# Kernel optimization log

Measured on AMD Instinct MI355X. Metric: run time of the kernel, lower is better.

The kernel has to match this reference:

```python
import jax, jax.numpy as jnp
import numpy as np

F_DIM = 128


def setup_inputs() -> dict:
    key = jax.random.key(0)
    ks = jax.random.split(key, 10)
    n_atoms = 50000
    n_edges = 500000
    F = F_DIM
    q = jax.random.normal(ks[0], (n_atoms, 1, F), dtype=jnp.float32)
    mu = jax.random.normal(ks[1], (n_atoms, 3, F), dtype=jnp.float32)
    Wij = jax.random.normal(ks[2], (n_edges, 1, 3 * F), dtype=jnp.float32)
    dir_ij = jax.random.normal(ks[3], (n_edges, 3), dtype=jnp.float32)
    idx_i = jax.random.randint(ks[4], (n_edges,), 0, n_atoms, dtype=jnp.int32)
    idx_j = jax.random.randint(ks[5], (n_edges,), 0, n_atoms, dtype=jnp.int32)
    # interatomic_context_net params: Dense(F,F,silu) -> Dense(F,3F)
    s1 = 1.0 / np.sqrt(F)
    W1 = jax.random.uniform(ks[6], (F, F), jnp.float32, -s1, s1)
    b1 = jax.random.uniform(ks[7], (F,), jnp.float32, -s1, s1)
    W2 = jax.random.uniform(ks[8], (F, 3 * F), jnp.float32, -s1, s1)
    b2 = jax.random.uniform(ks[9], (3 * F,), jnp.float32, -s1, s1)
    return {"q": q, "mu": mu, "Wij": Wij, "dir_ij": dir_ij,
            "W1": W1, "b1": b1, "W2": W2, "b2": b2,
            "idx_i": idx_i, "idx_j": idx_j, "n_atoms": n_atoms}


def reference(q, mu, Wij, dir_ij, W1, b1, W2, b2, idx_i, idx_j, n_atoms):
    F = F_DIM
    # context MLP on per-atom scalar features: [n_atoms, 1, 3F]
    h = jax.nn.silu(jnp.einsum('aif,fg->aig', q, W1) + b1)
    x = jnp.einsum('aif,fg->aig', h, W2) + b2
    # gather along edges
    xj = x[idx_j]          # [E, 1, 3F]
    muj = mu[idx_j]        # [E, 3, F]
    xw = Wij * xj          # [E, 1, 3F]
    dq, dmuR, dmumu = jnp.split(xw, 3, axis=-1)  # each [E, 1, F]
    dq_atom = jax.ops.segment_sum(dq, idx_i, num_segments=n_atoms)  # [n_atoms,1,F]
    dmu = dmuR * dir_ij[..., None] + dmumu * muj                    # [E,3,F]
    dmu_atom = jax.ops.segment_sum(dmu, idx_i, num_segments=n_atoms)
    return (q + dq_atom, mu + dmu_atom)
```

## Files before the change

### kernel.cpp

```cpp
#include <hip/hip_runtime.h>

typedef unsigned short u16;
typedef unsigned int   u32;

#define F 128
#define F3 384
#define TA 32
#define PAD 36

__device__ __forceinline__ float bf2f(u16 v) {
    union { u32 u; float f; } c; c.u = ((u32)v) << 16; return c.f;
}
__device__ __forceinline__ u16 f2bf(float f) {
    union { float fv; u32 u; } c; c.fv = f;
    u32 u = c.u;
    return (u16)((u + 0x7fffu + ((u >> 16) & 1u)) >> 16);
}

template<bool BF> __device__ __forceinline__ float LD(const void* p, size_t i) {
    return BF ? bf2f(((const u16*)p)[i]) : ((const float*)p)[i];
}
template<bool BF> __device__ __forceinline__ void ST(void* p, size_t i, float v) {
    if (BF) ((u16*)p)[i] = f2bf(v); else ((float*)p)[i] = v;
}
template<bool BF> __device__ __forceinline__ float2 LD2(const void* p, size_t i) {
    if (BF) {
        u32 v = *(const u32*)((const u16*)p + i);
        float2 r; r.x = bf2f((u16)(v & 0xffff)); r.y = bf2f((u16)(v >> 16)); return r;
    }
    return *(const float2*)((const float*)p + i);
}
template<bool BF> __device__ __forceinline__ void ST2(void* p, size_t i, float2 v) {
    if (BF) { *(u32*)((u16*)p + i) = ((u32)f2bf(v.y) << 16) | f2bf(v.x); }
    else    { *(float2*)((float*)p + i) = v; }
}
__device__ __forceinline__ float2 LD2bf(const u16* p, size_t i) {
    u32 v = *(const u32*)(p + i);
    float2 r; r.x = bf2f((u16)(v & 0xffff)); r.y = bf2f((u16)(v >> 16)); return r;
}
template<bool BF> __device__ __forceinline__ float4 LD4(const void* p, size_t i) {
    if (BF) {
        uint2 v = *(const uint2*)((const u16*)p + i);
        float4 r;
        r.x = bf2f((u16)(v.x & 0xffff)); r.y = bf2f((u16)(v.x >> 16));
        r.z = bf2f((u16)(v.y & 0xffff)); r.w = bf2f((u16)(v.y >> 16));
        return r;
    }
    return *(const float4*)((const float*)p + i);
}

__global__ __launch_bounds__(256) void detect_kernel(const void* q, int* flag) {
    __shared__ int cnt;
    if (threadIdx.x == 0) cnt = 0;
    __syncthreads();
    const u16* p = (const u16*)q;
    int c = 0;
    for (int i = threadIdx.x; i < 1024; i += 256) {
        u16 v = p[2 * i];
        int e = (v >> 7) & 0xFF;
        if (e >= 100 && e <= 150) c++;
    }
    atomicAdd(&cnt, c);
    __syncthreads();
    if (threadIdx.x == 0) *flag = (cnt > 512) ? 1 : 0;
}

template<bool BF>
__device__ void convmu_body(const void* mu, u16* dst, size_t n) {
    size_t i = ((size_t)blockIdx.x * 256 + threadIdx.x) * 8;
    if (i >= n) return;
    if (BF) {
        *(uint4*)(dst + i) = *(const uint4*)((const u16*)mu + i);
    } else {
        float4 a = *(const float4*)((const float*)mu + i);
        float4 b = *(const float4*)((const float*)mu + i + 4);
        uint4 o;
        o.x = ((u32)f2bf(a.y) << 16) | f2bf(a.x);
        o.y = ((u32)f2bf(a.w) << 16) | f2bf(a.z);
        o.z = ((u32)f2bf(b.y) << 16) | f2bf(b.x);
        o.w = ((u32)f2bf(b.w) << 16) | f2bf(b.z);
        *(uint4*)(dst + i) = o;
    }
}
__global__ __launch_bounds__(256) void convmu_kernel(const void* mu, u16* dst,
                                                     size_t n, const int* flag) {
    if (*flag) convmu_body<true >(mu, dst, n);
    else       convmu_body<false>(mu, dst, n);
}

template<bool BF>
__device__ void mlpfull_body(const void* q, const void* W1, const void* b1,
                             const void* W2, const void* b2,
                             u16* __restrict__ xcf, int n_atoms)
{
    __shared__ float qT[F][PAD];
    __shared__ float hT[F][PAD];

    const int tid = threadIdx.x;
    const int a0  = blockIdx.x * TA;
    const int c4  = (tid & 31) * 4;
    const int r4  = (tid >> 5) * 4;

    for (int i = tid; i < TA * F / 8; i += 256) {
        int a = i >> 4, f0 = (i & 15) * 8;
        float4 v0, v1;
        if (a0 + a < n_atoms) {
            v0 = LD4<BF>(q, (size_t)(a0 + a) * F + f0);
            v1 = LD4<BF>(q, (size_t)(a0 + a) * F + f0 + 4);
        } else { v0 = v1 = make_float4(0, 0, 0, 0); }
        qT[f0 + 0][a] = v0.x; qT[f0 + 1][a] = v0.y; qT[f0 + 2][a] = v0.z; qT[f0 + 3][a] = v0.w;
        qT[f0 + 4][a] = v1.x; qT[f0 + 5][a] = v1.y; qT[f0 + 6][a] = v1.z; qT[f0 + 7][a] = v1.w;
    }
    __syncthreads();

    {
        float acc[4][4];
#pragma unroll
        for (int rr = 0; rr < 4; ++rr)
#pragma unroll
            for (int cc = 0; cc < 4; ++cc) acc[rr][cc] = 0.0f;

        for (int f = 0; f < F; ++f) {
            float4 qv = *(const float4*)&qT[f][r4];
            float4 w  = LD4<BF>(W1, (size_t)f * F + c4);
            float qa[4] = {qv.x, qv.y, qv.z, qv.w};
            float wa[4] = {w.x, w.y, w.z, w.w};
#pragma unroll
            for (int rr = 0; rr < 4; ++rr)
#pragma unroll
                for (int cc = 0; cc < 4; ++cc)
                    acc[rr][cc] += qa[rr] * wa[cc];
        }
#pragma unroll
        for (int cc = 0; cc < 4; ++cc) {
            float bb = LD<BF>(b1, c4 + cc);
#pragma unroll
            for (int rr = 0; rr < 4; ++rr) {
                float h = acc[rr][cc] + bb;
                hT[c4 + cc][r4 + rr] = h / (1.0f + __expf(-h));
            }
        }
    }
    __syncthreads();

    for (int cb = 0; cb < 3; ++cb) {
        float acc[4][4];
#pragma unroll
        for (int rr = 0; rr < 4; ++rr)
#pragma unroll
            for (int cc = 0; cc < 4; ++cc) acc[rr][cc] = 0.0f;

        for (int f = 0; f < F; ++f) {
            float4 hv = *(const float4*)&hT[f][r4];
            float4 w  = LD4<BF>(W2, (size_t)f * F3 + cb * F + c4);
            float ha[4] = {hv.x, hv.y, hv.z, hv.w};
            float wa[4] = {w.x, w.y, w.z, w.w};
#pragma unroll
            for (int rr = 0; rr < 4; ++rr)
#pragma unroll
                for (int cc = 0; cc < 4; ++cc)
                    acc[rr][cc] += ha[rr] * wa[cc];
        }
        float bb[4];
#pragma unroll
        for (int cc = 0; cc < 4; ++cc) bb[cc] = LD<BF>(b2, cb * F + c4 + cc);
#pragma unroll
        for (int rr = 0; rr < 4; ++rr) {
            int ga = a0 + r4 + rr;
            if (ga < n_atoms) {
                uint2 o;
                o.x = ((u32)f2bf(acc[rr][1] + bb[1]) << 16) | f2bf(acc[rr][0] + bb[0]);
                o.y = ((u32)f2bf(acc[rr][3] + bb[3]) << 16) | f2bf(acc[rr][2] + bb[2]);
                *(uint2*)(xcf + (size_t)ga * F3 + cb * F + c4) = o;
            }
        }
    }
}
__global__ __launch_bounds__(256) void mlpfull_kernel(
    const void* q, const void* W1, const void* b1, const void* W2, const void* b2,
    u16* xcf, int n_atoms, const int* flag)
{
    if (*flag) mlpfull_body<true >(q, W1, b1, W2, b2, xcf, n_atoms);
    else       mlpfull_body<false>(q, W1, b1, W2, b2, xcf, n_atoms);
}

template<bool BF>
__device__ void mlp_body(const void* q, const void* W1, const void* b1,
                         const void* W2, const void* b2,
                         u16* __restrict__ xc, u16* __restrict__ hbuf,
                         int cb, int mode, int n_atoms)
{
    __shared__ float qT[F][PAD];
    __shared__ float hT[F][PAD];

    const int tid = threadIdx.x;
    const int a0  = blockIdx.x * TA;
    const int c4  = (tid & 31) * 4;
    const int r4  = (tid >> 5) * 4;

    if (mode == 2) {
        for (int i = tid; i < TA * F / 8; i += 256) {
            int a = i >> 4, f0 = (i & 15) * 8;
            float4 v0, v1;
            if (a0 + a < n_atoms) {
                v0 = LD4<true>(hbuf, (size_t)(a0 + a) * F + f0);
                v1 = LD4<true>(hbuf, (size_t)(a0 + a) * F + f0 + 4);
            } else { v0 = v1 = make_float4(0, 0, 0, 0); }
            hT[f0 + 0][a] = v0.x; hT[f0 + 1][a] = v0.y; hT[f0 + 2][a] = v0.z; hT[f0 + 3][a] = v0.w;
            hT[f0 + 4][a] = v1.x; hT[f0 + 5][a] = v1.y; hT[f0 + 6][a] = v1.z; hT[f0 + 7][a] = v1.w;
        }
        __syncthreads();
    } else {
        for (int i = tid; i < TA * F / 8; i += 256) {
            int a = i >> 4, f0 = (i & 15) * 8;
            float4 v0, v1;
            if (a0 + a < n_atoms) {
                v0 = LD4<BF>(q, (size_t)(a0 + a) * F + f0);
                v1 = LD4<BF>(q, (size_t)(a0 + a) * F + f0 + 4);
            } else { v0 = v1 = make_float4(0, 0, 0, 0); }
            qT[f0 + 0][a] = v0.x; qT[f0 + 1][a] = v0.y; qT[f0 + 2][a] = v0.z; qT[f0 + 3][a] = v0.w;
            qT[f0 + 4][a] = v1.x; qT[f0 + 5][a] = v1.y; qT[f0 + 6][a] = v1.z; qT[f0 + 7][a] = v1.w;
        }
        __syncthreads();

        float acc[4][4];
#pragma unroll
        for (int rr = 0; rr < 4; ++rr)
#pragma unroll
            for (int cc = 0; cc < 4; ++cc) acc[rr][cc] = 0.0f;

        for (int f = 0; f < F; ++f) {
            float4 qv = *(const float4*)&qT[f][r4];
            float4 w  = LD4<BF>(W1, (size_t)f * F + c4);
            float qa[4] = {qv.x, qv.y, qv.z, qv.w};
            float wa[4] = {w.x, w.y, w.z, w.w};
#pragma unroll
            for (int rr = 0; rr < 4; ++rr)
#pragma unroll
                for (int cc = 0; cc < 4; ++cc)
                    acc[rr][cc] += qa[rr] * wa[cc];
        }
        float hv[4][4];
#pragma unroll
        for (int cc = 0; cc < 4; ++cc) {
            float bb = LD<BF>(b1, c4 + cc);
#pragma unroll
            for (int rr = 0; rr < 4; ++rr) {
                float h = acc[rr][cc] + bb;
                float s = h / (1.0f + __expf(-h));
                hv[rr][cc] = s;
                hT[c4 + cc][r4 + rr] = s;
            }
        }
        if (mode == 1) {
#pragma unroll
            for (int rr = 0; rr < 4; ++rr) {
                int ga = a0 + r4 + rr;
                if (ga < n_atoms) {
                    *(u32*)(hbuf + (size_t)ga * F + c4)     = ((u32)f2bf(hv[rr][1]) << 16) | f2bf(hv[rr][0]);
                    *(u32*)(hbuf + (size_t)ga * F + c4 + 2) = ((u32)f2bf(hv[rr][3]) << 16) | f2bf(hv[rr][2]);
                }
            }
        }
        __syncthreads();
    }

    float acc[4][4];
#pragma unroll
    for (int rr = 0; rr < 4; ++rr)
#pragma unroll
        for (int cc = 0; cc < 4; ++cc) acc[rr][cc] = 0.0f;

    for (int f = 0; f < F; ++f) {
        float4 hv = *(const float4*)&hT[f][r4];
        float4 w  = LD4<BF>(W2, (size_t)f * F3 + cb * F + c4);
        float ha[4] = {hv.x, hv.y, hv.z, hv.w};
        float wa[4] = {w.x, w.y, w.z, w.w};
#pragma unroll
        for (int rr = 0; rr < 4; ++rr)
#pragma unroll
            for (int cc = 0; cc < 4; ++cc)
                acc[rr][cc] += ha[rr] * wa[cc];
    }
    float bb[4];
#pragma unroll
    for (int cc = 0; cc < 4; ++cc) bb[cc] = LD<BF>(b2, cb * F + c4 + cc);
#pragma unroll
    for (int rr = 0; rr < 4; ++rr) {
        int ga = a0 + r4 + rr;
        if (ga < n_atoms) {
            *(u32*)(xc + (size_t)ga * F + c4)     = ((u32)f2bf(acc[rr][1] + bb[1]) << 16) | f2bf(acc[rr][0] + bb[0]);
            *(u32*)(xc + (size_t)ga * F + c4 + 2) = ((u32)f2bf(acc[rr][3] + bb[3]) << 16) | f2bf(acc[rr][2] + bb[2]);
        }
    }
}
__global__ __launch_bounds__(256) void mlp_kernel(
    const void* q, const void* W1, const void* b1, const void* W2, const void* b2,
    u16* xc, u16* hbuf, int cb, int mode, int n_atoms, const int* flag)
{
    if (*flag) mlp_body<true >(q, W1, b1, W2, b2, xc, hbuf, cb, mode, n_atoms);
    else       mlp_body<false>(q, W1, b1, W2, b2, xc, hbuf, cb, mode, n_atoms);
}

__global__ __launch_bounds__(256) void count_kernel(
    const int* __restrict__ idx_i, int* __restrict__ counts, int E)
{
    int e = blockIdx.x * 256 + threadIdx.x;
    if (e < E) atomicAdd(&counts[idx_i[e]], 1);
}

__global__ __launch_bounds__(1024) void scan_kernel(
    const int* __restrict__ counts, int* __restrict__ offsets, int n)
{
    __shared__ int buf[1024];
    const int t = threadIdx.x;
    const int m = (n + 1023) >> 10;
    const int i0 = t * m;
    int s = 0;
    for (int r = 0; r < m; ++r) {
        int i = i0 + r;
        if (i < n) s += counts[i];
    }
    buf[t] = s;
    __syncthreads();
    for (int off = 1; off < 1024; off <<= 1) {
        int add = (t >= off) ? buf[t - off] : 0;
        __syncthreads();
        buf[t] += add;
        __syncthreads();
    }
    int run = buf[t] - s;
    for (int r = 0; r < m; ++r) {
        int i = i0 + r;
        if (i < n) { offsets[i] = run; run += counts[i]; }
    }
    if (t == 1023) offsets[n] = buf[1023];
}

__global__ __launch_bounds__(256) void scatter_kernel(
    const int* __restrict__ idx_i, const int* __restrict__ offsets,
    int* __restrict__ cursor, int* __restrict__ perm, int E)
{
    int e = blockIdx.x * 256 + threadIdx.x;
    if (e < E) {
        int i = idx_i[e];
        int pos = offsets[i] + atomicAdd(&cursor[i], 1);
        perm[pos] = e;
    }
}

template<bool BF>
__device__ void gfused_body(const void* q, const void* mu, const void* Wij,
                            const void* dir, const u16* __restrict__ xcf,
                            const u16* __restrict__ mubf,
                            const int* __restrict__ idx_j,
                            const int* __restrict__ offsets,
                            const int* __restrict__ perm,
                            void* out, int n_atoms, int E)
{
    int a    = blockIdx.x * 4 + (threadIdx.x >> 6);
    int lane = threadIdx.x & 63;
    if (a >= n_atoms) return;
    const size_t fo = 2 * lane;
    const size_t ob = (size_t)n_atoms * F;

    float2 sq = LD2<BF>(q, (size_t)a * F + fo);
    float2 s0 = LD2<BF>(mu, (size_t)a * F3 + fo);
    float2 s1 = LD2<BF>(mu, (size_t)a * F3 + 128 + fo);
    float2 s2 = LD2<BF>(mu, (size_t)a * F3 + 256 + fo);

    int k0 = offsets[a], k1 = offsets[a + 1];
    for (int kb = k0; kb < k1; kb += 64) {
        int cnt = k1 - kb; if (cnt > 64) cnt = 64;
        int e_r = 0, j_r = 0;
        if (lane < cnt) {
            e_r = perm[kb + lane]; if ((unsigned)e_r >= (unsigned)E) e_r = 0;
            j_r = idx_j[e_r];      if ((unsigned)j_r >= (unsigned)n_atoms) j_r = 0;
        }
#pragma unroll 2
        for (int c = 0; c < cnt; ++c) {
            int e = __shfl(e_r, c, 64);
            int j = __shfl(j_r, c, 64);
            const size_t wb = (size_t)e * F3;
            const size_t jb = (size_t)j * F3;
            float2 wq = LD2<BF>(Wij, wb + fo);
            float2 wR = LD2<BF>(Wij, wb + 128 + fo);
            float2 wm = LD2<BF>(Wij, wb + 256 + fo);
            float2 xq = LD2bf(xcf, jb + fo);
            float2 xR = LD2bf(xcf, jb + 128 + fo);
            float2 xm = LD2bf(xcf, jb + 256 + fo);
            float2 m0 = LD2bf(mubf, jb + fo);
            float2 m1 = LD2bf(mubf, jb + 128 + fo);
            float2 m2 = LD2bf(mubf, jb + 256 + fo);
            float d0 = LD<BF>(dir, (size_t)e * 3 + 0);
            float d1 = LD<BF>(dir, (size_t)e * 3 + 1);
            float d2 = LD<BF>(dir, (size_t)e * 3 + 2);

            sq.x += wq.x * xq.x;           sq.y += wq.y * xq.y;
            float tR0 = wR.x * xR.x,  tR1 = wR.y * xR.y;
            float tm0 = wm.x * xm.x,  tm1 = wm.y * xm.y;
            s0.x += tR0 * d0 + tm0 * m0.x; s0.y += tR1 * d0 + tm1 * m0.y;
            s1.x += tR0 * d1 + tm0 * m1.x; s1.y += tR1 * d1 + tm1 * m1.y;
            s2.x += tR0 * d2 + tm0 * m2.x; s2.y += tR1 * d2 + tm1 * m2.y;
        }
    }
    ST2<BF>(out, (size_t)a * F + fo, sq);
    ST2<BF>(out, ob + (size_t)a * F3 + fo,       s0);
    ST2<BF>(out, ob + (size_t)a * F3 + 128 + fo, s1);
    ST2<BF>(out, ob + (size_t)a * F3 + 256 + fo, s2);
}
__global__ __launch_bounds__(256) void gfused_kernel(
    const void* q, const void* mu, const void* Wij, const void* dir,
    const u16* xcf, const u16* mubf, const int* idx_j, const int* offsets,
    const int* perm, void* out, int n_atoms, int E, const int* flag)
{
    if (*flag) gfused_body<true >(q, mu, Wij, dir, xcf, mubf, idx_j, offsets, perm, out, n_atoms, E);
    else       gfused_body<false>(q, mu, Wij, dir, xcf, mubf, idx_j, offsets, perm, out, n_atoms, E);
}

template<bool BF>
__device__ void gq_body(const void* q, const void* Wij, const u16* __restrict__ xc,
                        const int* __restrict__ idx_j, const int* __restrict__ offsets,
                        const int* __restrict__ perm, void* out, int n_atoms, int E)
{
    int a    = blockIdx.x * 4 + (threadIdx.x >> 6);
    int lane = threadIdx.x & 63;
    if (a >= n_atoms) return;
    const size_t fo = 2 * lane;

    float2 s = LD2<BF>(q, (size_t)a * F + fo);
    int k0 = offsets[a], k1 = offsets[a + 1];
    for (int kb = k0; kb < k1; kb += 64) {
        int cnt = k1 - kb; if (cnt > 64) cnt = 64;
        int e_r = 0, j_r = 0;
        if (lane < cnt) {
            e_r = perm[kb + lane]; if ((unsigned)e_r >= (unsigned)E) e_r = 0;
            j_r = idx_j[e_r];      if ((unsigned)j_r >= (unsigned)n_atoms) j_r = 0;
        }
        for (int c = 0; c < cnt; ++c) {
            int e = __shfl(e_r, c, 64);
            int j = __shfl(j_r, c, 64);
            float2 w  = LD2<BF>(Wij, (size_t)e * F3 + fo);
            float2 xv = LD2bf(xc, (size_t)j * F + fo);
            s.x += w.x * xv.x;
            s.y += w.y * xv.y;
        }
    }
    ST2<BF>(out, (size_t)a * F + fo, s);
}
__global__ __launch_bounds__(256) void gather_q_kernel(
    const void* q, const void* Wij, const u16* xc, const int* idx_j,
    const int* offsets, const int* perm, void* out, int n_atoms, int E, const int* flag)
{
    if (*flag) gq_body<true >(q, Wij, xc, idx_j, offsets, perm, out, n_atoms, E);
    else       gq_body<false>(q, Wij, xc, idx_j, offsets, perm, out, n_atoms, E);
}

template<bool BF, int MODE>
__device__ void gmu_body(const void* mu, const void* Wij, const void* dir,
                         const u16* __restrict__ xc, const int* __restrict__ idx_j,
                         const int* __restrict__ offsets, const int* __restrict__ perm,
                         void* out, int n_atoms, int E)
{
    int a    = blockIdx.x * 4 + (threadIdx.x >> 6);
    int lane = threadIdx.x & 63;
    if (a >= n_atoms) return;
    const size_t fo = 2 * lane;
    const size_t ob = (size_t)n_atoms * F;

    float2 s0, s1, s2;
    if (MODE == 1) {
        s0 = LD2<BF>(mu, (size_t)a * F3 + fo);
        s1 = LD2<BF>(mu, (size_t)a * F3 + 128 + fo);
        s2 = LD2<BF>(mu, (size_t)a * F3 + 256 + fo);
    } else {
        s0 = LD2<BF>(out, ob + (size_t)a * F3 + fo);
        s1 = LD2<BF>(out, ob + (size_t)a * F3 + 128 + fo);
        s2 = LD2<BF>(out, ob + (size_t)a * F3 + 256 + fo);
    }

    const int wofs = (MODE == 1) ? 128 : 256;
    int k0 = offsets[a], k1 = offsets[a + 1];
    for (int kb = k0; kb < k1; kb += 64) {
        int cnt = k1 - kb; if (cnt > 64) cnt = 64;
        int e_r = 0, j_r = 0;
        if (lane < cnt) {
            e_r = perm[kb + lane]; if ((unsigned)e_r >= (unsigned)E) e_r = 0;
            j_r = idx_j[e_r];      if ((unsigned)j_r >= (unsigned)n_atoms) j_r = 0;
        }
        for (int c = 0; c < cnt; ++c) {
            int e = __shfl(e_r, c, 64);
            int j = __shfl(j_r, c, 64);
            float2 w  = LD2<BF>(Wij, (size_t)e * F3 + wofs + fo);
            float2 xv = LD2bf(xc, (size_t)j * F + fo);
            float wx0 = w.x * xv.x, wx1 = w.y * xv.y;
            if (MODE == 1) {
                float d0 = LD<BF>(dir, (size_t)e * 3 + 0);
                float d1 = LD<BF>(dir, (size_t)e * 3 + 1);
                float d2 = LD<BF>(dir, (size_t)e * 3 + 2);
                s0.x += wx0 * d0; s0.y += wx1 * d0;
                s1.x += wx0 * d1; s1.y += wx1 * d1;
                s2.x += wx0 * d2; s2.y += wx1 * d2;
            } else {
                float2 m0 = LD2<BF>(mu, (size_t)j * F3 + fo);
                float2 m1 = LD2<BF>(mu, (size_t)j * F3 + 128 + fo);
                float2 m2 = LD2<BF>(mu, (size_t)j * F3 + 256 + fo);
                s0.x += wx0 * m0.x; s0.y += wx1 * m0.y;
                s1.x += wx0 * m1.x; s1.y += wx1 * m1.y;
                s2.x += wx0 * m2.x; s2.y += wx1 * m2.y;
            }
        }
    }
    ST2<BF>(out, ob + (size_t)a * F3 + fo,       s0);
    ST2<BF>(out, ob + (size_t)a * F3 + 128 + fo, s1);
    ST2<BF>(out, ob + (size_t)a * F3 + 256 + fo, s2);
}
__global__ __launch_bounds__(256) void gather_mu_kernel(
    const void* mu, const void* Wij, const void* dir, const u16* xc,
    const int* idx_j, const int* offsets, const int* perm, void* out,
    int n_atoms, int E, int mode, const int* flag)
{
    if (*flag) {
        if (mode == 1) gmu_body<true, 1>(mu, Wij, dir, xc, idx_j, offsets, perm, out, n_atoms, E);
        else           gmu_body<true, 2>(mu, Wij, dir, xc, idx_j, offsets, perm, out, n_atoms, E);
    } else {
        if (mode == 1) gmu_body<false, 1>(mu, Wij, dir, xc, idx_j, offsets, perm, out, n_atoms, E);
        else           gmu_body<false, 2>(mu, Wij, dir, xc, idx_j, offsets, perm, out, n_atoms, E);
    }
}

extern "C" void kernel_launch(void* const* d_in, const int* in_sizes, int n_in,
                              void* d_out, int out_size, void* d_ws, size_t ws_size,
                              hipStream_t stream)
{
    const void* q   = d_in[0];
    const void* mu  = d_in[1];
    const void* Wij = d_in[2];
    const void* dir = d_in[3];
    const void* W1  = d_in[4];
    const void* b1  = d_in[5];
    const void* W2  = d_in[6];
    const void* b2  = d_in[7];
    const int* idx_i = (const int*)d_in[8];
    const int* idx_j = (const int*)d_in[9];

    const int n_atoms = in_sizes[0] / F;
    const int E       = in_sizes[8];
    const int eBlocks = (E + 255) / 256;
    const int gBlocks = (n_atoms + 3) / 4;
    const int mlpBlocks = (n_atoms + TA - 1) / TA;

    {
        u16* xcf     = (u16*)d_ws;
        u16* mubf    = xcf + (size_t)n_atoms * F3;
        int* flag    = (int*)(mubf + (size_t)n_atoms * F3);
        int* counts  = flag + 4;
        int* cursor  = counts + n_atoms;
        int* offsets = cursor + n_atoms;
        int* perm    = offsets + n_atoms + 1;
        size_t need  = (size_t)((char*)(perm + E) - (char*)d_ws);

        if (ws_size >= need) {
            detect_kernel<<<1, 256, 0, stream>>>(q, flag);
            hipMemsetAsync(counts, 0, (size_t)2 * n_atoms * sizeof(int), stream);
            count_kernel<<<eBlocks, 256, 0, stream>>>(idx_i, counts, E);
            scan_kernel<<<1, 1024, 0, stream>>>(counts, offsets, n_atoms);
            scatter_kernel<<<eBlocks, 256, 0, stream>>>(idx_i, offsets, cursor, perm, E);

            size_t nmu = (size_t)n_atoms * F3;
            convmu_kernel<<<(int)((nmu / 8 + 255) / 256), 256, 0, stream>>>(mu, mubf, nmu, flag);
            mlpfull_kernel<<<mlpBlocks, 256, 0, stream>>>(q, W1, b1, W2, b2, xcf, n_atoms, flag);

            gfused_kernel<<<gBlocks, 256, 0, stream>>>(q, mu, Wij, dir, xcf, mubf,
                                                       idx_j, offsets, perm, d_out,
                                                       n_atoms, E, flag);
            return;
        }
    }

    u16* xc      = (u16*)d_ws;
    int* flag    = (int*)(xc + (size_t)n_atoms * F);
    int* counts  = flag + 4;
    int* cursor  = counts + n_atoms;
    int* offsets = cursor + n_atoms;
    int* perm    = offsets + n_atoms + 1;
    u16* hbuf    = (u16*)(perm + E);
    size_t need_h = (size_t)((char*)(hbuf + (size_t)n_atoms * F) - (char*)d_ws);
    const bool useH = (ws_size >= need_h);

    detect_kernel<<<1, 256, 0, stream>>>(q, flag);
    hipMemsetAsync(counts, 0, (size_t)2 * n_atoms * sizeof(int), stream);
    count_kernel<<<eBlocks, 256, 0, stream>>>(idx_i, counts, E);
    scan_kernel<<<1, 1024, 0, stream>>>(counts, offsets, n_atoms);
    scatter_kernel<<<eBlocks, 256, 0, stream>>>(idx_i, offsets, cursor, perm, E);

    mlp_kernel<<<mlpBlocks, 256, 0, stream>>>(q, W1, b1, W2, b2, xc, hbuf, 0,
                                              useH ? 1 : 0, n_atoms, flag);
    gather_q_kernel<<<gBlocks, 256, 0, stream>>>(q, Wij, xc, idx_j, offsets, perm,
                                                 d_out, n_atoms, E, flag);
    mlp_kernel<<<mlpBlocks, 256, 0, stream>>>(q, W1, b1, W2, b2, xc, hbuf, 1,
                                              useH ? 2 : 0, n_atoms, flag);
    gather_mu_kernel<<<gBlocks, 256, 0, stream>>>(mu, Wij, dir, xc, idx_j, offsets, perm,
                                                  d_out, n_atoms, E, 1, flag);
    mlp_kernel<<<mlpBlocks, 256, 0, stream>>>(q, W1, b1, W2, b2, xc, hbuf, 2,
                                              useH ? 2 : 0, n_atoms, flag);
    gather_mu_kernel<<<gBlocks, 256, 0, stream>>>(mu, Wij, dir, xc, idx_j, offsets, perm,
                                                  d_out, n_atoms, E, 2, flag);
}
```

Measured before the change: 605.0 us.

## Interleave gathered per-atom features into 4-wide bf16 layout for single 16B loads

The MLP output and the bf16 copy of mu are stored interleaved per feature (three channels padded to four), so each lane in the gather kernel fetches one 16-byte vector per source atom instead of six 4-byte loads. The edge direction loads are moved to a per-batch lane load plus shuffles, and edge weights and outputs use nontemporal loads and stores. The gather loop unroll factor goes from 2 to 4. The padding adds a third more workspace and gather traffic for these buffers, and the conversion kernel now reads mu with strided scalar loads.

```diff
diff --git a/kernel.cpp b/kernel.cpp
--- a/kernel.cpp
+++ b/kernel.cpp
@@ -2,6 +2,7 @@
 
 typedef unsigned short u16;
 typedef unsigned int   u32;
+typedef unsigned long long u64;
 
 #define F 128
 #define F3 384
@@ -16,12 +17,15 @@
     u32 u = c.u;
     return (u16)((u + 0x7fffu + ((u >> 16) & 1u)) >> 16);
 }
+__device__ __forceinline__ float u2f(u32 v) {
+    union { u32 u; float f; } c; c.u = v; return c.f;
+}
+__device__ __forceinline__ u32 f2u(float v) {
+    union { float f; u32 u; } c; c.f = v; return c.u;
+}
 
 template<bool BF> __device__ __forceinline__ float LD(const void* p, size_t i) {
     return BF ? bf2f(((const u16*)p)[i]) : ((const float*)p)[i];
-}
-template<bool BF> __device__ __forceinline__ void ST(void* p, size_t i, float v) {
-    if (BF) ((u16*)p)[i] = f2bf(v); else ((float*)p)[i] = v;
 }
 template<bool BF> __device__ __forceinline__ float2 LD2(const void* p, size_t i) {
     if (BF) {
@@ -47,6 +51,24 @@
         return r;
     }
     return *(const float4*)((const float*)p + i);
+}
+template<bool BF> __device__ __forceinline__ float2 NTLD2(const void* p, size_t i) {
+    if (BF) {
+        u32 v = __builtin_nontemporal_load((const u32*)((const u16*)p + i));
+        float2 r; r.x = bf2f((u16)(v & 0xffff)); r.y = bf2f((u16)(v >> 16)); return r;
+    } else {
+        u64 v = __builtin_nontemporal_load((const u64*)((const float*)p + i));
+        float2 r; r.x = u2f((u32)v); r.y = u2f((u32)(v >> 32)); return r;
+    }
+}
+template<bool BF> __device__ __forceinline__ void NTST2(void* p, size_t i, float2 v) {
+    if (BF) {
+        u32 o = ((u32)f2bf(v.y) << 16) | f2bf(v.x);
+        __builtin_nontemporal_store(o, (u32*)((u16*)p + i));
+    } else {
+        u64 o = ((u64)f2u(v.y) << 32) | f2u(v.x);
+        __builtin_nontemporal_store(o, (u64*)((float*)p + i));
+    }
 }
 
 __global__ __launch_bounds__(256) void detect_kernel(const void* q, int* flag) {
@@ -66,32 +88,28 @@
 }
 
 template<bool BF>
-__device__ void convmu_body(const void* mu, u16* dst, size_t n) {
-    size_t i = ((size_t)blockIdx.x * 256 + threadIdx.x) * 8;
-    if (i >= n) return;
-    if (BF) {
-        *(uint4*)(dst + i) = *(const uint4*)((const u16*)mu + i);
-    } else {
-        float4 a = *(const float4*)((const float*)mu + i);
-        float4 b = *(const float4*)((const float*)mu + i + 4);
-        uint4 o;
-        o.x = ((u32)f2bf(a.y) << 16) | f2bf(a.x);
-        o.y = ((u32)f2bf(a.w) << 16) | f2bf(a.z);
-        o.z = ((u32)f2bf(b.y) << 16) | f2bf(b.x);
-        o.w = ((u32)f2bf(b.w) << 16) | f2bf(b.z);
-        *(uint4*)(dst + i) = o;
-    }
-}
-__global__ __launch_bounds__(256) void convmu_kernel(const void* mu, u16* dst,
-                                                     size_t n, const int* flag) {
-    if (*flag) convmu_body<true >(mu, dst, n);
-    else       convmu_body<false>(mu, dst, n);
+__device__ void mu4_body(const void* mu, u16* dst, int n_atoms) {
+    int a = blockIdx.x * 2 + (threadIdx.x >> 7);
+    int f = threadIdx.x & 127;
+    if (a >= n_atoms) return;
+    float m0 = LD<BF>(mu, (size_t)a * F3 + f);
+    float m1 = LD<BF>(mu, (size_t)a * F3 + 128 + f);
+    float m2 = LD<BF>(mu, (size_t)a * F3 + 256 + f);
+    uint2 o;
+    o.x = ((u32)f2bf(m1) << 16) | f2bf(m0);
+    o.y = f2bf(m2);
+    *(uint2*)(dst + ((size_t)a * F + f) * 4) = o;
+}
+__global__ __launch_bounds__(256) void mu4_kernel(const void* mu, u16* dst,
+                                                  int n_atoms, const int* flag) {
+    if (*flag) mu4_body<true >(mu, dst, n_atoms);
+    else       mu4_body<false>(mu, dst, n_atoms);
 }
 
 template<bool BF>
 __device__ void mlpfull_body(const void* q, const void* W1, const void* b1,
                              const void* W2, const void* b2,
-                             u16* __restrict__ xcf, int n_atoms)
+                             u16* __restrict__ xcf4, int n_atoms)
 {
     __shared__ float qT[F][PAD];
     __shared__ float hT[F][PAD];
@@ -143,6 +161,8 @@
     }
     __syncthreads();
 
+    float xout[4][4][3];
+#pragma unroll
     for (int cb = 0; cb < 3; ++cb) {
         float acc[4][4];
 #pragma unroll
@@ -161,27 +181,162 @@
                 for (int cc = 0; cc < 4; ++cc)
                     acc[rr][cc] += ha[rr] * wa[cc];
         }
-        float bb[4];
-#pragma unroll
-        for (int cc = 0; cc < 4; ++cc) bb[cc] = LD<BF>(b2, cb * F + c4 + cc);
-#pragma unroll
-        for (int rr = 0; rr < 4; ++rr) {
-            int ga = a0 + r4 + rr;
-            if (ga < n_atoms) {
-                uint2 o;
-                o.x = ((u32)f2bf(acc[rr][1] + bb[1]) << 16) | f2bf(acc[rr][0] + bb[0]);
-                o.y = ((u32)f2bf(acc[rr][3] + bb[3]) << 16) | f2bf(acc[rr][2] + bb[2]);
-                *(uint2*)(xcf + (size_t)ga * F3 + cb * F + c4) = o;
-            }
+#pragma unroll
+        for (int cc = 0; cc < 4; ++cc) {
+            float bb = LD<BF>(b2, cb * F + c4 + cc);
+#pragma unroll
+            for (int rr = 0; rr < 4; ++rr)
+                xout[rr][cc][cb] = acc[rr][cc] + bb;
+        }
+    }
+#pragma unroll
+    for (int rr = 0; rr < 4; ++rr) {
+        int ga = a0 + r4 + rr;
+        if (ga < n_atoms) {
+            uint4 o1, o2;
+            o1.x = ((u32)f2bf(xout[rr][0][1]) << 16) | f2bf(xout[rr][0][0]);
+            o1.y = f2bf(xout[rr][0][2]);
+            o1.z = ((u32)f2bf(xout[rr][1][1]) << 16) | f2bf(xout[rr][1][0]);
+            o1.w = f2bf(xout[rr][1][2]);
+            o2.x = ((u32)f2bf(xout[rr][2][1]) << 16) | f2bf(xout[rr][2][0]);
+            o2.y = f2bf(xout[rr][2][2]);
+            o2.z = ((u32)f2bf(xout[rr][3][1]) << 16) | f2bf(xout[rr][3][0]);
+            o2.w = f2bf(xout[rr][3][2]);
+            *(uint4*)(xcf4 + ((size_t)ga * F + c4) * 4)     = o1;
+            *(uint4*)(xcf4 + ((size_t)ga * F + c4) * 4 + 8) = o2;
         }
     }
 }
 __global__ __launch_bounds__(256) void mlpfull_kernel(
     const void* q, const void* W1, const void* b1, const void* W2, const void* b2,
-    u16* xcf, int n_atoms, const int* flag)
-{
-    if (*flag) mlpfull_body<true >(q, W1, b1, W2, b2, xcf, n_atoms);
-    else       mlpfull_body<false>(q, W1, b1, W2, b2, xcf, n_atoms);
+    u16* xcf4, int n_atoms, const int* flag)
+{
+    if (*flag) mlpfull_body<true >(q, W1, b1, W2, b2, xcf4, n_atoms);
+    else       mlpfull_body<false>(q, W1, b1, W2, b2, xcf4, n_atoms);
+}
+
+__global__ __launch_bounds__(256) void count_kernel(
+    const int* __restrict__ idx_i, int* __restrict__ counts, int E)
+{
+    int e = blockIdx.x * 256 + threadIdx.x;
+    if (e < E) atomicAdd(&counts[idx_i[e]], 1);
+}
+
+__global__ __launch_bounds__(1024) void scan_kernel(
+    const int* __restrict__ counts, int* __restrict__ offsets, int n)
+{
+    __shared__ int buf[1024];
+    const int t = threadIdx.x;
+    const int m = (n + 1023) >> 10;
+    const int i0 = t * m;
+    int s = 0;
+    for (int r = 0; r < m; ++r) {
+        int i = i0 + r;
+        if (i < n) s += counts[i];
+    }
+    buf[t] = s;
+    __syncthreads();
+    for (int off = 1; off < 1024; off <<= 1) {
+        int add = (t >= off) ? buf[t - off] : 0;
+        __syncthreads();
+        buf[t] += add;
+        __syncthreads();
+    }
+    int run = buf[t] - s;
+    for (int r = 0; r < m; ++r) {
+        int i = i0 + r;
+        if (i < n) { offsets[i] = run; run += counts[i]; }
+    }
+    if (t == 1023) offsets[n] = buf[1023];
+}
+
+__global__ __launch_bounds__(256) void scatter_kernel(
+    const int* __restrict__ idx_i, const int* __restrict__ offsets,
+    int* __restrict__ cursor, int* __restrict__ perm, int E)
+{
+    int e = blockIdx.x * 256 + threadIdx.x;
+    if (e < E) {
+        int i = idx_i[e];
+        int pos = offsets[i] + atomicAdd(&cursor[i], 1);
+        perm[pos] = e;
+    }
+}
+
+template<bool BF>
+__device__ void gfused_body(const void* q, const void* mu, const void* Wij,
+                            const void* dir, const u16* __restrict__ xcf4,
+                            const u16* __restrict__ mubf4,
+                            const int* __restrict__ idx_j,
+                            const int* __restrict__ offsets,
+                            const int* __restrict__ perm,
+                            void* out, int n_atoms, int E)
+{
+    int a    = blockIdx.x * 4 + (threadIdx.x >> 6);
+    int lane = threadIdx.x & 63;
+    if (a >= n_atoms) return;
+    const size_t fo = 2 * lane;
+    const size_t ob = (size_t)n_atoms * F;
+
+    float2 sq = LD2<BF>(q, (size_t)a * F + fo);
+    float2 s0 = LD2<BF>(mu, (size_t)a * F3 + fo);
+    float2 s1 = LD2<BF>(mu, (size_t)a * F3 + 128 + fo);
+    float2 s2 = LD2<BF>(mu, (size_t)a * F3 + 256 + fo);
+
+    int k0 = offsets[a], k1 = offsets[a + 1];
+    for (int kb = k0; kb < k1; kb += 64) {
+        int cnt = k1 - kb; if (cnt > 64) cnt = 64;
+        int e_r = 0, j_r = 0;
+        float d0_r = 0.0f, d1_r = 0.0f, d2_r = 0.0f;
+        if (lane < cnt) {
+            e_r = perm[kb + lane]; if ((unsigned)e_r >= (unsigned)E) e_r = 0;
+            j_r = idx_j[e_r];      if ((unsigned)j_r >= (unsigned)n_atoms) j_r = 0;
+            d0_r = LD<BF>(dir, (size_t)e_r * 3 + 0);
+            d1_r = LD<BF>(dir, (size_t)e_r * 3 + 1);
+            d2_r = LD<BF>(dir, (size_t)e_r * 3 + 2);
+        }
+#pragma unroll 4
+        for (int c = 0; c < cnt; ++c) {
+            int   e  = __shfl(e_r, c, 64);
+            int   j  = __shfl(j_r, c, 64);
+            float d0 = __shfl(d0_r, c, 64);
+            float d1 = __shfl(d1_r, c, 64);
+            float d2 = __shfl(d2_r, c, 64);
+
+            float2 wq = NTLD2<BF>(Wij, (size_t)e * F3 + fo);
+            float2 wR = NTLD2<BF>(Wij, (size_t)e * F3 + 128 + fo);
+            float2 wm = NTLD2<BF>(Wij, (size_t)e * F3 + 256 + fo);
+            uint4 xv = *(const uint4*)(xcf4  + (size_t)j * 512 + 8 * (size_t)lane);
+            uint4 mv = *(const uint4*)(mubf4 + (size_t)j * 512 + 8 * (size_t)lane);
+
+            float xq0 = bf2f((u16)(xv.x & 0xffff)), xR0 = bf2f((u16)(xv.x >> 16));
+            float xm0 = bf2f((u16)(xv.y & 0xffff));
+            float xq1 = bf2f((u16)(xv.z & 0xffff)), xR1 = bf2f((u16)(xv.z >> 16));
+            float xm1 = bf2f((u16)(xv.w & 0xffff));
+            float m00 = bf2f((u16)(mv.x & 0xffff)), m01 = bf2f((u16)(mv.x >> 16));
+            float m02 = bf2f((u16)(mv.y & 0xffff));
+            float m10 = bf2f((u16)(mv.z & 0xffff)), m11 = bf2f((u16)(mv.z >> 16));
+            float m12 = bf2f((u16)(mv.w & 0xffff));
+
+            sq.x += wq.x * xq0;  sq.y += wq.y * xq1;
+            float tR0 = wR.x * xR0, tR1 = wR.y * xR1;
+            float tm0 = wm.x * xm0, tm1 = wm.y * xm1;
+            s0.x += tR0 * d0 + tm0 * m00;  s0.y += tR1 * d0 + tm1 * m10;
+            s1.x += tR0 * d1 + tm0 * m01;  s1.y += tR1 * d1 + tm1 * m11;
+            s2.x += tR0 * d2 + tm0 * m02;  s2.y += tR1 * d2 + tm1 * m12;
+        }
+    }
+    NTST2<BF>(out, (size_t)a * F + fo, sq);
+    NTST2<BF>(out, ob + (size_t)a * F3 + fo,       s0);
+    NTST2<BF>(out, ob + (size_t)a * F3 + 128 + fo, s1);
+    NTST2<BF>(out, ob + (size_t)a * F3 + 256 + fo, s2);
+}
+__global__ __launch_bounds__(256) void gfused_kernel(
+    const void* q, const void* mu, const void* Wij, const void* dir,
+    const u16* xcf4, const u16* mubf4, const int* idx_j, const int* offsets,
+    const int* perm, void* out, int n_atoms, int E, const int* flag)
+{
+    if (*flag) gfused_body<true >(q, mu, Wij, dir, xcf4, mubf4, idx_j, offsets, perm, out, n_atoms, E);
+    else       gfused_body<false>(q, mu, Wij, dir, xcf4, mubf4, idx_j, offsets, perm, out, n_atoms, E);
 }
 
 template<bool BF>
@@ -300,122 +455,6 @@
 {
     if (*flag) mlp_body<true >(q, W1, b1, W2, b2, xc, hbuf, cb, mode, n_atoms);
     else       mlp_body<false>(q, W1, b1, W2, b2, xc, hbuf, cb, mode, n_atoms);
-}
-
-__global__ __launch_bounds__(256) void count_kernel(
-    const int* __restrict__ idx_i, int* __restrict__ counts, int E)
-{
-    int e = blockIdx.x * 256 + threadIdx.x;
-    if (e < E) atomicAdd(&counts[idx_i[e]], 1);
-}
-
-__global__ __launch_bounds__(1024) void scan_kernel(
-    const int* __restrict__ counts, int* __restrict__ offsets, int n)
-{
-    __shared__ int buf[1024];
-    const int t = threadIdx.x;
-    const int m = (n + 1023) >> 10;
-    const int i0 = t * m;
-    int s = 0;
-    for (int r = 0; r < m; ++r) {
-        int i = i0 + r;
-        if (i < n) s += counts[i];
-    }
-    buf[t] = s;
-    __syncthreads();
-    for (int off = 1; off < 1024; off <<= 1) {
-        int add = (t >= off) ? buf[t - off] : 0;
-        __syncthreads();
-        buf[t] += add;
-        __syncthreads();
-    }
-    int run = buf[t] - s;
-    for (int r = 0; r < m; ++r) {
-        int i = i0 + r;
-        if (i < n) { offsets[i] = run; run += counts[i]; }
-    }
-    if (t == 1023) offsets[n] = buf[1023];
-}
-
-__global__ __launch_bounds__(256) void scatter_kernel(
-    const int* __restrict__ idx_i, const int* __restrict__ offsets,
-    int* __restrict__ cursor, int* __restrict__ perm, int E)
-{
-    int e = blockIdx.x * 256 + threadIdx.x;
-    if (e < E) {
-        int i = idx_i[e];
-        int pos = offsets[i] + atomicAdd(&cursor[i], 1);
-        perm[pos] = e;
-    }
-}
-
-template<bool BF>
-__device__ void gfused_body(const void* q, const void* mu, const void* Wij,
-                            const void* dir, const u16* __restrict__ xcf,
-                            const u16* __restrict__ mubf,
-                            const int* __restrict__ idx_j,
-                            const int* __restrict__ offsets,
-                            const int* __restrict__ perm,
-                            void* out, int n_atoms, int E)
-{
-    int a    = blockIdx.x * 4 + (threadIdx.x >> 6);
-    int lane = threadIdx.x & 63;
-    if (a >= n_atoms) return;
-    const size_t fo = 2 * lane;
-    const size_t ob = (size_t)n_atoms * F;
-
-    float2 sq = LD2<BF>(q, (size_t)a * F + fo);
-    float2 s0 = LD2<BF>(mu, (size_t)a * F3 + fo);
-    float2 s1 = LD2<BF>(mu, (size_t)a * F3 + 128 + fo);
-    float2 s2 = LD2<BF>(mu, (size_t)a * F3 + 256 + fo);
-
-    int k0 = offsets[a], k1 = offsets[a + 1];
-    for (int kb = k0; kb < k1; kb += 64) {
-        int cnt = k1 - kb; if (cnt > 64) cnt = 64;
-        int e_r = 0, j_r = 0;
-        if (lane < cnt) {
-            e_r = perm[kb + lane]; if ((unsigned)e_r >= (unsigned)E) e_r = 0;
-            j_r = idx_j[e_r];      if ((unsigned)j_r >= (unsigned)n_atoms) j_r = 0;
-        }
-#pragma unroll 2
-        for (int c = 0; c < cnt; ++c) {
-            int e = __shfl(e_r, c, 64);
-            int j = __shfl(j_r, c, 64);
-            const size_t wb = (size_t)e * F3;
-            const size_t jb = (size_t)j * F3;
-            float2 wq = LD2<BF>(Wij, wb + fo);
-            float2 wR = LD2<BF>(Wij, wb + 128 + fo);
-            float2 wm = LD2<BF>(Wij, wb + 256 + fo);
-            float2 xq = LD2bf(xcf, jb + fo);
-            float2 xR = LD2bf(xcf, jb + 128 + fo);
-            float2 xm = LD2bf(xcf, jb + 256 + fo);
-            float2 m0 = LD2bf(mubf, jb + fo);
-            float2 m1 = LD2bf(mubf, jb + 128 + fo);
-            float2 m2 = LD2bf(mubf, jb + 256 + fo);
-            float d0 = LD<BF>(dir, (size_t)e * 3 + 0);
-            float d1 = LD<BF>(dir, (size_t)e * 3 + 1);
-            float d2 = LD<BF>(dir, (size_t)e * 3 + 2);
-
-            sq.x += wq.x * xq.x;           sq.y += wq.y * xq.y;
-            float tR0 = wR.x * xR.x,  tR1 = wR.y * xR.y;
-            float tm0 = wm.x * xm.x,  tm1 = wm.y * xm.y;
-            s0.x += tR0 * d0 + tm0 * m0.x; s0.y += tR1 * d0 + tm1 * m0.y;
-            s1.x += tR0 * d1 + tm0 * m1.x; s1.y += tR1 * d1 + tm1 * m1.y;
-            s2.x += tR0 * d2 + tm0 * m2.x; s2.y += tR1 * d2 + tm1 * m2.y;
-        }
-    }
-    ST2<BF>(out, (size_t)a * F + fo, sq);
-    ST2<BF>(out, ob + (size_t)a * F3 + fo,       s0);
-    ST2<BF>(out, ob + (size_t)a * F3 + 128 + fo, s1);
-    ST2<BF>(out, ob + (size_t)a * F3 + 256 + fo, s2);
-}
-__global__ __launch_bounds__(256) void gfused_kernel(
-    const void* q, const void* mu, const void* Wij, const void* dir,
-    const u16* xcf, const u16* mubf, const int* idx_j, const int* offsets,
-    const int* perm, void* out, int n_atoms, int E, const int* flag)
-{
-    if (*flag) gfused_body<true >(q, mu, Wij, dir, xcf, mubf, idx_j, offsets, perm, out, n_atoms, E);
-    else       gfused_body<false>(q, mu, Wij, dir, xcf, mubf, idx_j, offsets, perm, out, n_atoms, E);
 }
 
 template<bool BF>
@@ -551,9 +590,9 @@
     const int mlpBlocks = (n_atoms + TA - 1) / TA;
 
     {
-        u16* xcf     = (u16*)d_ws;
-        u16* mubf    = xcf + (size_t)n_atoms * F3;
-        int* flag    = (int*)(mubf + (size_t)n_atoms * F3);
+        u16* xcf4    = (u16*)d_ws;
+        u16* mubf4   = xcf4 + (size_t)n_atoms * F * 4;
+        int* flag    = (int*)(mubf4 + (size_t)n_atoms * F * 4);
         int* counts  = flag + 4;
         int* cursor  = counts + n_atoms;
         int* offsets = cursor + n_atoms;
@@ -567,11 +606,10 @@
             scan_kernel<<<1, 1024, 0, stream>>>(counts, offsets, n_atoms);
             scatter_kernel<<<eBlocks, 256, 0, stream>>>(idx_i, offsets, cursor, perm, E);
 
-            size_t nmu = (size_t)n_atoms * F3;
-            convmu_kernel<<<(int)((nmu / 8 + 255) / 256), 256, 0, stream>>>(mu, mubf, nmu, flag);
-            mlpfull_kernel<<<mlpBlocks, 256, 0, stream>>>(q, W1, b1, W2, b2, xcf, n_atoms, flag);
-
-            gfused_kernel<<<gBlocks, 256, 0, stream>>>(q, mu, Wij, dir, xcf, mubf,
+            mu4_kernel<<<(n_atoms + 1) / 2, 256, 0, stream>>>(mu, mubf4, n_atoms, flag);
+            mlpfull_kernel<<<mlpBlocks, 256, 0, stream>>>(q, W1, b1, W2, b2, xcf4, n_atoms, flag);
+
+            gfused_kernel<<<gBlocks, 256, 0, stream>>>(q, mu, Wij, dir, xcf4, mubf4,
                                                        idx_j, offsets, perm, d_out,
                                                        n_atoms, E, flag);
             return;
```

Measured after the change: 608.2 us. About the same (+0.5%).
